# Kernel optimization log

Hardware: AMD Instinct MI355X
Metric: run time of the kernel (lower is better)

The kernel has to match this reference:

```python
import jax, jax.numpy as jnp
import numpy as np

D_MODEL = 2048
N_HEAD = 16
HEAD_DIM = D_MODEL // N_HEAD


def setup_inputs() -> dict:
    key = jax.random.key(0)
    k1, k2, k3 = jax.random.split(key, 3)
    B, T = 4, 1024
    x = jax.random.normal(k1, (B, T, D_MODEL), dtype=jnp.float32)
    # Linear(d_model, 3*d_model, bias=False): stored as [in, out] for x @ W
    w_qkv = jax.random.normal(k2, (D_MODEL, 3 * D_MODEL), dtype=jnp.float32) * (1.0 / np.sqrt(D_MODEL))
    w_proj = jax.random.normal(k3, (D_MODEL, D_MODEL), dtype=jnp.float32) * (1.0 / np.sqrt(D_MODEL))
    return {"x": x, "w_qkv": w_qkv, "w_proj": w_proj}


def reference(x, w_qkv, w_proj):
    B, T, C = x.shape
    H, Dh = N_HEAD, HEAD_DIM
    qkv = x @ w_qkv                              # [B, T, 3C]
    q, k, v = jnp.split(qkv, 3, axis=-1)
    # [B, T, C] -> [B, H, T, Dh]
    q = q.reshape(B, T, H, Dh).transpose(0, 2, 1, 3)
    k = k.reshape(B, T, H, Dh).transpose(0, 2, 1, 3)
    v = v.reshape(B, T, H, Dh).transpose(0, 2, 1, 3)
    scale = 1.0 / np.sqrt(Dh).astype(np.float32)
    scores = jnp.einsum('bhqd,bhkd->bhqk', q, k) * scale   # [B, H, T, T]
    causal = jnp.tril(jnp.ones((T, T), dtype=bool))
    scores = jnp.where(causal, scores, jnp.finfo(scores.dtype).min)
    attn = jax.nn.softmax(scores, axis=-1)
    y = jnp.einsum('bhqk,bhkd->bhqd', attn, v)             # [B, H, T, Dh]
    y = y.transpose(0, 2, 1, 3).reshape(B, T, C)
    return y @ w_proj
```

## Files before the change

### kernel.cpp

```cpp
#include <hip/hip_runtime.h>
#include <cstdint>
#include <cstddef>


typedef __attribute__((ext_vector_type(8))) __bf16 bf16x8;
typedef __attribute__((ext_vector_type(4))) float f32x4;
typedef unsigned short u16;

#define NEG_BIG (-1.0e30f)

__device__ __forceinline__ u16 f2bf(float f) {
    union { float f; uint32_t u; } v; v.f = f;
    uint32_t r = v.u + 0x7FFFu + ((v.u >> 16) & 1u);
    return (u16)(r >> 16);
}

__device__ __forceinline__ uint32_t pack2(float a, float b) {
    return (uint32_t)f2bf(a) | ((uint32_t)f2bf(b) << 16);
}

__device__ __forceinline__ f32x4 mfma16(bf16x8 a, bf16x8 b, f32x4 c) {
    return __builtin_amdgcn_mfma_f32_16x16x32_bf16(a, b, c, 0, 0, 0);
}

__device__ __forceinline__ void async16(const u16* g, u16* l) {
    __builtin_amdgcn_global_load_lds(
        (const __attribute__((address_space(1))) void*)g,
        (__attribute__((address_space(3))) void*)l, 16, 0, 0);
}

__global__ __launch_bounds__(256) void cvt_bf16(
    const float* __restrict__ x, u16* __restrict__ xb) {
    size_t i = ((size_t)blockIdx.x * 256 + threadIdx.x) * 8;
    float4 u = *(const float4*)(x + i);
    float4 v = *(const float4*)(x + i + 4);
    uint4 p;
    p.x = pack2(u.x, u.y); p.y = pack2(u.z, u.w);
    p.z = pack2(v.x, v.y); p.w = pack2(v.z, v.w);
    *(uint4*)(xb + i) = p;
}

__global__ __launch_bounds__(256) void transpose_w(
    const float* __restrict__ W, int ldW, u16* __restrict__ WT) {
    __shared__ u16 tile[64][68];
    const int n0 = blockIdx.x * 64, k0 = blockIdx.y * 64;
    const int t = threadIdx.x;
    for (int i = t; i < 4096; i += 256) {
        int r = i >> 6, c = i & 63;
        tile[r][c] = f2bf(W[(size_t)(k0 + r) * ldW + n0 + c]);
    }
    __syncthreads();
    for (int i = t; i < 4096; i += 256) {
        int r = i >> 6, c = i & 63;
        WT[(size_t)(n0 + r) * 2048 + k0 + c] = tile[c][r];
    }
}

__global__ __launch_bounds__(256) void gemm_k(
    const void* __restrict__ Av, const u16* __restrict__ Bt,
    int N, int amode, int omode,
    float* __restrict__ outf, u16* __restrict__ Qo, u16* __restrict__ Ko,
    u16* __restrict__ Vt) {
    const int K = 2048;
    __shared__ u16 As[128][32];
    __shared__ u16 Bs[128][32];

    const float* A32 = (const float*)Av;
    const u16*   A16 = (const u16*)Av;

    const int m0 = blockIdx.y * 128, n0 = blockIdx.x * 128;
    const int t = threadIdx.x;
    const int w = t >> 6, lane = t & 63;
    const int col = lane & 15, quad = lane >> 4;
    const int wrow = (w >> 1) * 64, wcol = (w & 1) * 64;

    f32x4 acc[4][4];
    #pragma unroll
    for (int i = 0; i < 4; ++i)
        #pragma unroll
        for (int j = 0; j < 4; ++j)
            acc[i][j] = (f32x4){0.f, 0.f, 0.f, 0.f};

    u16* as_flat = &As[0][0];
    u16* bs_flat = &Bs[0][0];
    const int c1 = (w << 6) | lane;
    const int c2 = c1 + 256;

    for (int k0 = 0; k0 < K; k0 += 32) {
        {
            const u16* g1 = Bt + (size_t)(n0 + (c1 >> 2)) * K + k0 + ((c1 & 3) << 3);
            async16(g1, bs_flat + (size_t)w * 512);
            const u16* g2 = Bt + (size_t)(n0 + (c2 >> 2)) * K + k0 + ((c2 & 3) << 3);
            async16(g2, bs_flat + 2048 + (size_t)w * 512);
        }
        if (amode == 2) {
            const u16* g1 = A16 + (size_t)(m0 + (c1 >> 2)) * K + k0 + ((c1 & 3) << 3);
            async16(g1, as_flat + (size_t)w * 512);
            const u16* g2 = A16 + (size_t)(m0 + (c2 >> 2)) * K + k0 + ((c2 & 3) << 3);
            async16(g2, as_flat + 2048 + (size_t)w * 512);
        } else if (amode == 1) {
            #pragma unroll
            for (int cc = 0; cc < 2; ++cc) {
                int c = cc ? c2 : c1;
                int r = c >> 2, ko = (c & 3) << 3;
                int kg = k0 + ko, h = kg >> 7, d = kg & 127;
                int m = m0 + r, b = m >> 10, tt = m & 1023;
                const u16* g = A16 + (((size_t)(b * 16 + h)) * 1024 + tt) * 128 + d;
                async16(g, as_flat + (size_t)(cc ? 2048 : 0) + (size_t)w * 512);
            }
        } else if (amode == 0) {
            #pragma unroll
            for (int c = t; c < 512; c += 256) {
                int r = c >> 2, ko = (c & 3) * 8;
                size_t off = (size_t)(m0 + r) * K + k0 + ko;
                float4 u = *(const float4*)(A32 + off);
                float4 v = *(const float4*)(A32 + off + 4);
                uint4 p;
                p.x = pack2(u.x, u.y); p.y = pack2(u.z, u.w);
                p.z = pack2(v.x, v.y); p.w = pack2(v.z, v.w);
                *(uint4*)&As[r][ko] = p;
            }
        } else {
            #pragma unroll
            for (int c = t; c < 512; c += 256) {
                int r = c >> 2, ko = (c & 3) * 8;
                int kg = k0 + ko, h = kg >> 7, d = kg & 127;
                int m = m0 + r, b = m >> 10, tt = m & 1023;
                *(uint4*)&As[r][ko] =
                    *(const uint4*)(A16 + (((size_t)(b * 16 + h)) * 1024 + tt) * 128 + d);
            }
        }
        __syncthreads();

        bf16x8 afr[4], bfr[4];
        #pragma unroll
        for (int i = 0; i < 4; ++i)
            afr[i] = *(const bf16x8*)&As[wrow + i * 16 + col][quad * 8];
        #pragma unroll
        for (int i = 0; i < 4; ++i)
            bfr[i] = *(const bf16x8*)&Bs[wcol + i * 16 + col][quad * 8];

        #pragma unroll
        for (int mt = 0; mt < 4; ++mt)
            #pragma unroll
            for (int nt = 0; nt < 4; ++nt)
                acc[mt][nt] = mfma16(afr[mt], bfr[nt], acc[mt][nt]);
        __syncthreads();
    }

    #pragma unroll
    for (int mt = 0; mt < 4; ++mt) {
        #pragma unroll
        for (int nt = 0; nt < 4; ++nt) {
            #pragma unroll
            for (int r = 0; r < 4; ++r) {
                int gm = m0 + wrow + mt * 16 + quad * 4 + r;
                int gn = n0 + wcol + nt * 16 + col;
                if (omode == 0) {
                    outf[(size_t)gm * N + gn] = acc[mt][nt][r];
                } else {
                    u16 bv = f2bf(acc[mt][nt][r]);
                    int b = gm >> 10, tq = gm & 1023;
                    if (omode == 3) {
                        int which = gn >> 11, rem = gn & 2047;
                        int h = rem >> 7, d = rem & 127;
                        size_t bh = (size_t)b * 16 + h;
                        if (which == 0)      Qo[(bh * 1024 + tq) * 128 + d] = bv;
                        else if (which == 1) Ko[(bh * 1024 + tq) * 128 + d] = bv;
                        else                 Vt[(bh * 128 + d) * 1024 + tq] = bv;
                    } else {
                        int h = gn >> 7, d = gn & 127;
                        size_t bh = (size_t)b * 16 + h;
                        if (omode == 1) Qo[(bh * 1024 + tq) * 128 + d] = bv;
                        else            Vt[(bh * 128 + d) * 1024 + tq] = bv;
                    }
                }
            }
        }
    }
}

__device__ __forceinline__ bf16x8 ldsfrag(const u16* buf, int row, int ksl, int quad) {
    return *(const bf16x8*)(buf + (size_t)row * 64 +
                            ((((ksl << 2) | quad) ^ (row & 7)) << 3));
}

template<int AMODE>
__device__ __forceinline__ void stageA(
    u16* halfb, const u16* A, int m0h, int k0, int w, int lane) {
    #pragma unroll
    for (int j = 0; j < 2; ++j) {
        int s0 = (j << 9) | (w << 6);
        int s = s0 + lane;
        int r = s >> 3;
        int gc = (s & 7) ^ (r & 7);
        int k = k0 + (gc << 3);
        const u16* src;
        if constexpr (AMODE == 2) {
            src = A + (size_t)(m0h + r) * 2048 + k;
        } else {
            int m = m0h + r, b = m >> 10, tt = m & 1023;
            int hh = k >> 7, d = k & 127;
            src = A + (((size_t)(b * 16 + hh)) * 1024 + tt) * 128 + d;
        }
        async16(src, halfb + (size_t)s0 * 8);
    }
}

__device__ __forceinline__ void stageB256(
    u16* halfb, const u16* Bt, int n0h, int k0, int w, int lane) {
    #pragma unroll
    for (int j = 0; j < 2; ++j) {
        int s0 = (j << 9) | (w << 6);
        int s = s0 + lane;
        int r = s >> 3;
        int gc = (s & 7) ^ (r & 7);
        async16(Bt + (size_t)(n0h + r) * 2048 + k0 + (gc << 3),
                halfb + (size_t)s0 * 8);
    }
}

template<int AMODE, int OMODE>
__global__ __launch_bounds__(512, 2) void gemm256(
    const u16* __restrict__ A, const u16* __restrict__ Bt, int N,
    float* __restrict__ outf, u16* __restrict__ Qo, u16* __restrict__ Ko,
    u16* __restrict__ Vt) {
    __shared__ u16 As[2][256 * 64];
    __shared__ u16 Bs[2][256 * 64];

    const int m0 = blockIdx.y * 256, n0 = blockIdx.x * 256;
    const int t = threadIdx.x;
    const int w = t >> 6, lane = t & 63;
    const int col = lane & 15, quad = lane >> 4;
    const int wr16 = ((w >> 2) & 1) << 4;
    const int wc16 = (w & 3) << 4;

    f32x4 acc[8][4];
    #pragma unroll
    for (int i = 0; i < 8; ++i)
        #pragma unroll
        for (int j = 0; j < 4; ++j)
            acc[i][j] = (f32x4){0.f, 0.f, 0.f, 0.f};

    stageA<AMODE>(As[0],             A,  m0,       0, w, lane);
    stageB256(    Bs[0],             Bt, n0,       0, w, lane);
    stageB256(    Bs[0] + 128 * 64,  Bt, n0 + 128, 0, w, lane);
    stageA<AMODE>(As[0] + 128 * 64,  A,  m0 + 128, 0, w, lane);
    asm volatile("s_waitcnt vmcnt(4)" ::: "memory");
    __builtin_amdgcn_s_barrier();

    const int NT = 2048 / 64;
    bf16x8 a_frag[8], b0_frag[4], b1_frag[4];

    for (int kt = 0; kt < NT; ++kt) {
        const int bt = kt & 1, bn = bt ^ 1;
        const int ktn = (kt + 1 < NT) ? kt + 1 : 0;
        const u16* asC = As[bt];
        const u16* bsC = Bs[bt];
        u16* asN = As[bn];
        u16* bsN = Bs[bn];
        const int kN = ktn * 64;

        #pragma unroll
        for (int mr = 0; mr < 4; ++mr)
            #pragma unroll
            for (int ks = 0; ks < 2; ++ks)
                a_frag[mr * 2 + ks] = ldsfrag(asC, mr * 32 + wr16 + col, ks, quad);
        #pragma unroll
        for (int nr = 0; nr < 2; ++nr)
            #pragma unroll
            for (int ks = 0; ks < 2; ++ks)
                b0_frag[nr * 2 + ks] = ldsfrag(bsC, nr * 64 + wc16 + col, ks, quad);
        stageA<AMODE>(asN, A, m0, kN, w, lane);
        asm volatile("s_waitcnt vmcnt(4)" ::: "memory");
        __builtin_amdgcn_s_barrier();
        __builtin_amdgcn_s_setprio(1);
        #pragma unroll
        for (int mr = 0; mr < 4; ++mr)
            #pragma unroll
            for (int nr = 0; nr < 2; ++nr)
                #pragma unroll
                for (int ks = 0; ks < 2; ++ks)
                    acc[mr][nr] = mfma16(a_frag[mr * 2 + ks], b0_frag[nr * 2 + ks], acc[mr][nr]);
        __builtin_amdgcn_s_setprio(0);

        #pragma unroll
        for (int nr = 0; nr < 2; ++nr)
            #pragma unroll
            for (int ks = 0; ks < 2; ++ks)
                b1_frag[nr * 2 + ks] = ldsfrag(bsC, (nr + 2) * 64 + wc16 + col, ks, quad);
        stageB256(bsN, Bt, n0, kN, w, lane);
        asm volatile("s_waitcnt vmcnt(4)" ::: "memory");
        __builtin_amdgcn_s_barrier();
        __builtin_amdgcn_s_setprio(1);
        #pragma unroll
        for (int mr = 0; mr < 4; ++mr)
            #pragma unroll
            for (int nr = 0; nr < 2; ++nr)
                #pragma unroll
                for (int ks = 0; ks < 2; ++ks)
                    acc[mr][nr + 2] = mfma16(a_frag[mr * 2 + ks], b1_frag[nr * 2 + ks], acc[mr][nr + 2]);
        __builtin_amdgcn_s_setprio(0);

        #pragma unroll
        for (int mr = 0; mr < 4; ++mr)
            #pragma unroll
            for (int ks = 0; ks < 2; ++ks)
                a_frag[mr * 2 + ks] = ldsfrag(asC, (mr + 4) * 32 + wr16 + col, ks, quad);
        stageB256(bsN + 128 * 64, Bt, n0 + 128, kN, w, lane);
        __builtin_amdgcn_s_barrier();
        __builtin_amdgcn_s_setprio(1);
        #pragma unroll
        for (int mr = 0; mr < 4; ++mr)
            #pragma unroll
            for (int nr = 0; nr < 2; ++nr)
                #pragma unroll
                for (int ks = 0; ks < 2; ++ks)
                    acc[mr + 4][nr + 2] = mfma16(a_frag[mr * 2 + ks], b1_frag[nr * 2 + ks], acc[mr + 4][nr + 2]);
        __builtin_amdgcn_s_setprio(0);

        stageA<AMODE>(asN + 128 * 64, A, m0 + 128, kN, w, lane);
        asm volatile("s_waitcnt vmcnt(4)" ::: "memory");
        __builtin_amdgcn_s_barrier();
        __builtin_amdgcn_s_setprio(1);
        #pragma unroll
        for (int mr = 0; mr < 4; ++mr)
            #pragma unroll
            for (int nr = 0; nr < 2; ++nr)
                #pragma unroll
                for (int ks = 0; ks < 2; ++ks)
                    acc[mr + 4][nr] = mfma16(a_frag[mr * 2 + ks], b0_frag[nr * 2 + ks], acc[mr + 4][nr]);
        __builtin_amdgcn_s_setprio(0);
    }

    #pragma unroll
    for (int mr = 0; mr < 8; ++mr) {
        #pragma unroll
        for (int nr = 0; nr < 4; ++nr) {
            #pragma unroll
            for (int r = 0; r < 4; ++r) {
                int gm = m0 + mr * 32 + wr16 + quad * 4 + r;
                int gn = n0 + nr * 64 + wc16 + col;
                if constexpr (OMODE == 0) {
                    outf[(size_t)gm * N + gn] = acc[mr][nr][r];
                } else {
                    u16 bv = f2bf(acc[mr][nr][r]);
                    int b = gm >> 10, tq = gm & 1023;
                    int which = gn >> 11, rem = gn & 2047;
                    int hh = rem >> 7, d = rem & 127;
                    size_t bh = (size_t)b * 16 + hh;
                    if (which == 0)      Qo[(bh * 1024 + tq) * 128 + d] = bv;
                    else if (which == 1) Ko[(bh * 1024 + tq) * 128 + d] = bv;
                    else                 Vt[(bh * 128 + d) * 1024 + tq] = bv;
                }
            }
        }
    }
}

__global__ __launch_bounds__(256) void attn_kernel(
    u16* __restrict__ Q, const u16* __restrict__ K,
    const u16* __restrict__ VT) {
    __shared__ u16 Ks[64 * 128];
    __shared__ u16 Vs[128 * 64];
    __shared__ u16 Ps[4][16][68];

    const int qb = (int)(gridDim.x - 1) - (int)blockIdx.x;
    const int h = blockIdx.y, b = blockIdx.z;
    const int t = threadIdx.x;
    const int w = t >> 6, lane = t & 63;
    const int col = lane & 15, quad = lane >> 4;
    const int sw = col & 7;
    const size_t bh = (size_t)b * 16 + h;
    u16* Qb = Q + bh * (1024 * 128);
    const u16* Kb = K + bh * (1024 * 128);
    const u16* Vb = VT + bh * (128 * 1024);
    const int q_lane = qb * 64 + w * 16 + col;

    bf16x8 qf[4];
    {
        const u16* qp = Qb + (size_t)q_lane * 128 + quad * 8;
        #pragma unroll
        for (int kq = 0; kq < 4; ++kq)
            qf[kq] = *(const bf16x8*)(qp + kq * 32);
    }

    f32x4 o[8];
    #pragma unroll
    for (int i = 0; i < 8; ++i) o[i] = (f32x4){0.f, 0.f, 0.f, 0.f};
    float m = NEG_BIG, l = 0.f;
    const float scale = 0.08838834764831845f;

    for (int kt = 0; kt <= qb; ++kt) {
        const u16* Kt = Kb + (size_t)kt * (64 * 128);

        #pragma unroll
        for (int i = 0; i < 4; ++i) {
            int s = i * 256 + w * 64 + lane;
            int kr = s >> 4, kc = s & 15;
            async16(Kt + (size_t)kr * 128 + ((kc ^ (kr & 7)) << 3),
                    Ks + (size_t)(i * 256 + w * 64) * 8);
            int vr = s >> 3, vc = s & 7;
            async16(Vb + (size_t)vr * 1024 + kt * 64 + ((vc ^ (vr & 7)) << 3),
                    Vs + (size_t)(i * 256 + w * 64) * 8);
        }
        __syncthreads();

        const bool need_mask = (kt == qb);
        const int ttmax = need_mask ? w : 3;
        f32x4 s[4];
        #pragma unroll
        for (int tt = 0; tt < 4; ++tt) {
            if (tt > ttmax) { s[tt] = (f32x4){NEG_BIG, NEG_BIG, NEG_BIG, NEG_BIG}; continue; }
            const u16* kbase = Ks + (size_t)(tt * 16 + col) * 128;
            f32x4 a = (f32x4){0.f, 0.f, 0.f, 0.f};
            #pragma unroll
            for (int kq = 0; kq < 4; ++kq)
                a = mfma16(*(const bf16x8*)(kbase + (((kq * 4 + quad) ^ sw) << 3)),
                           qf[kq], a);
            s[tt] = a;
        }

        float rmax = NEG_BIG;
        #pragma unroll
        for (int tt = 0; tt < 4; ++tt) {
            if (tt > ttmax) continue;
            #pragma unroll
            for (int r = 0; r < 4; ++r) {
                float v = s[tt][r] * scale;
                int tg = kt * 64 + tt * 16 + quad * 4 + r;
                if (need_mask && tg > q_lane) v = NEG_BIG;
                s[tt][r] = v;
                rmax = fmaxf(rmax, v);
            }
        }
        rmax = fmaxf(rmax, __shfl_xor(rmax, 16, 64));
        rmax = fmaxf(rmax, __shfl_xor(rmax, 32, 64));

        float mnew = fmaxf(m, rmax);
        float alpha = __expf(m - mnew);
        m = mnew;

        float rsum = 0.f;
        #pragma unroll
        for (int tt = 0; tt < 4; ++tt) {
            uint32_t* dst = (uint32_t*)&Ps[w][col][tt * 16 + quad * 4];
            if (tt > ttmax) { dst[0] = 0u; dst[1] = 0u; continue; }
            float p0 = __expf(s[tt][0] - mnew);
            float p1 = __expf(s[tt][1] - mnew);
            float p2 = __expf(s[tt][2] - mnew);
            float p3 = __expf(s[tt][3] - mnew);
            rsum += (p0 + p1) + (p2 + p3);
            dst[0] = pack2(p0, p1);
            dst[1] = pack2(p2, p3);
        }
        rsum += __shfl_xor(rsum, 16, 64);
        rsum += __shfl_xor(rsum, 32, 64);
        l = l * alpha + rsum;

        #pragma unroll
        for (int dt = 0; dt < 8; ++dt)
            #pragma unroll
            for (int r = 0; r < 4; ++r) o[dt][r] *= alpha;

        #pragma unroll
        for (int ks = 0; ks < 2; ++ks) {
            bf16x8 pf = *(const bf16x8*)&Ps[w][col][ks * 32 + quad * 8];
            #pragma unroll
            for (int dt = 0; dt < 8; ++dt) {
                const u16* vbase = Vs + (size_t)(dt * 16 + col) * 64;
                o[dt] = mfma16(*(const bf16x8*)(vbase + (((ks * 4 + quad) ^ sw) << 3)),
                               pf, o[dt]);
            }
        }
        __syncthreads();
    }

    float inv = 1.0f / l;
    #pragma unroll
    for (int dt = 0; dt < 8; ++dt) {
        uint2 p;
        p.x = pack2(o[dt][0] * inv, o[dt][1] * inv);
        p.y = pack2(o[dt][2] * inv, o[dt][3] * inv);
        *(uint2*)&Qb[(size_t)q_lane * 128 + dt * 16 + quad * 4] = p;
    }
}

extern "C" void kernel_launch(void* const* d_in, const int* in_sizes, int n_in,
                              void* d_out, int out_size, void* d_ws, size_t ws_size,
                              hipStream_t stream) {
    const float* x      = (const float*)d_in[0];
    const float* w_qkv  = (const float*)d_in[1];
    const float* w_proj = (const float*)d_in[2];
    float* out = (float*)d_out;

    const size_t SEG = (size_t)4 * 16 * 1024 * 128;
    const size_t NEED_FAST = ((size_t)6144 * 2048 + SEG * 4) * 2;

    if (ws_size >= NEED_FAST + (1u << 20)) {
        u16* wT = (u16*)d_ws;
        u16* xb = wT + (size_t)6144 * 2048;
        u16* Qb = xb + SEG;
        u16* Kb = Qb + SEG;
        u16* Vb = Kb + SEG;

        cvt_bf16<<<4096, 256, 0, stream>>>(x, xb);
        transpose_w<<<dim3(96, 32), 256, 0, stream>>>(w_qkv, 6144, wT);

        gemm256<2, 3><<<dim3(24, 16), 512, 0, stream>>>(xb, wT, 6144,
                                                        nullptr, Qb, Kb, Vb);

        attn_kernel<<<dim3(16, 16, 4), 256, 0, stream>>>(Qb, Kb, Vb);

        transpose_w<<<dim3(32, 32), 256, 0, stream>>>(w_proj, 2048, wT);
        gemm_k<<<dim3(16, 32), 256, 0, stream>>>(Qb, wT, 2048, 1, 0,
                                                 out, nullptr, nullptr, nullptr);
    } else {
        u16* wT = (u16*)d_ws;
        u16* Qb = wT + (size_t)2048 * 2048;
        u16* Kb = Qb + SEG;
        u16* Vb = Kb + SEG;

        transpose_w<<<dim3(32, 32), 256, 0, stream>>>(w_qkv + 0, 6144, wT);
        gemm_k<<<dim3(16, 32), 256, 0, stream>>>(x, wT, 2048, 0, 1,
                                                 nullptr, Qb, nullptr, nullptr);
        transpose_w<<<dim3(32, 32), 256, 0, stream>>>(w_qkv + 2048, 6144, wT);
        gemm_k<<<dim3(16, 32), 256, 0, stream>>>(x, wT, 2048, 0, 1,
                                                 nullptr, Kb, nullptr, nullptr);
        transpose_w<<<dim3(32, 32), 256, 0, stream>>>(w_qkv + 4096, 6144, wT);
        gemm_k<<<dim3(16, 32), 256, 0, stream>>>(x, wT, 2048, 0, 2,
                                                 nullptr, nullptr, nullptr, Vb);

        attn_kernel<<<dim3(16, 16, 4), 256, 0, stream>>>(Qb, Kb, Vb);

        transpose_w<<<dim3(32, 32), 256, 0, stream>>>(w_proj, 2048, wT);
        gemm_k<<<dim3(16, 32), 256, 0, stream>>>(Qb, wT, 2048, 3, 0,
                                                 out, nullptr, nullptr, nullptr);
    }
}
```

Measured before the change: 437.8 us.

## Restructure GEMM main loop into quarter-buffer ping-pong pipeline with deeper prefetch

Splits the LDS A/B tiles into 128-row halves and unrolls the K loop by two, with a 'zigzag' order of 8 MFMA quadrants per iteration. Each quadrant's shared-memory half is refilled by async loads as soon as it has been consumed. The prologue prefetches most of the next K tile, so more global loads stay in flight (vmcnt 6) and fewer stalls land on barriers. The risk is tricky hazards in buffer reuse, and the final B half seems to rely on wrap-around indexing.

```diff
diff --git a/kernel.cpp b/kernel.cpp
--- a/kernel.cpp
+++ b/kernel.cpp
@@ -185,6 +185,37 @@
                             ((((ksl << 2) | quad) ^ (row & 7)) << 3));
 }
 
+__device__ __forceinline__ void read_a(bf16x8* af, const u16* buf,
+                                       int wr16, int col, int quad) {
+    #pragma unroll
+    for (int mr = 0; mr < 4; ++mr)
+        #pragma unroll
+        for (int ks = 0; ks < 2; ++ks)
+            af[mr * 2 + ks] = ldsfrag(buf, mr * 32 + wr16 + col, ks, quad);
+}
+
+__device__ __forceinline__ void read_b(bf16x8* bf, const u16* buf,
+                                       int wc16, int col, int quad) {
+    #pragma unroll
+    for (int nr = 0; nr < 2; ++nr)
+        #pragma unroll
+        for (int ks = 0; ks < 2; ++ks)
+            bf[nr * 2 + ks] = ldsfrag(buf, nr * 64 + wc16 + col, ks, quad);
+}
+
+__device__ __forceinline__ void mfma8(f32x4 (&acc)[8][4], int mh, int nh,
+                                      const bf16x8* af, const bf16x8* bf) {
+    #pragma unroll
+    for (int mr = 0; mr < 4; ++mr)
+        #pragma unroll
+        for (int nr = 0; nr < 2; ++nr)
+            #pragma unroll
+            for (int ks = 0; ks < 2; ++ks)
+                acc[mh * 4 + mr][nh * 2 + nr] =
+                    mfma16(af[mr * 2 + ks], bf[nr * 2 + ks],
+                           acc[mh * 4 + mr][nh * 2 + nr]);
+}
+
 template<int AMODE>
 __device__ __forceinline__ void stageA(
     u16* halfb, const u16* A, int m0h, int k0, int w, int lane) {
@@ -225,8 +256,8 @@
     const u16* __restrict__ A, const u16* __restrict__ Bt, int N,
     float* __restrict__ outf, u16* __restrict__ Qo, u16* __restrict__ Ko,
     u16* __restrict__ Vt) {
-    __shared__ u16 As[2][256 * 64];
-    __shared__ u16 Bs[2][256 * 64];
+    __shared__ u16 As[2][2][128 * 64];
+    __shared__ u16 Bs[2][2][128 * 64];
 
     const int m0 = blockIdx.y * 256, n0 = blockIdx.x * 256;
     const int t = threadIdx.x;
@@ -242,94 +273,82 @@
         for (int j = 0; j < 4; ++j)
             acc[i][j] = (f32x4){0.f, 0.f, 0.f, 0.f};
 
-    stageA<AMODE>(As[0],             A,  m0,       0, w, lane);
-    stageB256(    Bs[0],             Bt, n0,       0, w, lane);
-    stageB256(    Bs[0] + 128 * 64,  Bt, n0 + 128, 0, w, lane);
-    stageA<AMODE>(As[0] + 128 * 64,  A,  m0 + 128, 0, w, lane);
-    asm volatile("s_waitcnt vmcnt(4)" ::: "memory");
+    stageA<AMODE>(As[0][0], A,  m0,       0,  w, lane);
+    stageB256(    Bs[0][1], Bt, n0 + 128, 0,  w, lane);
+    stageA<AMODE>(As[0][1], A,  m0 + 128, 0,  w, lane);
+    stageB256(    Bs[0][0], Bt, n0,       0,  w, lane);
+    stageA<AMODE>(As[1][0], A,  m0,       64, w, lane);
+    stageB256(    Bs[1][1], Bt, n0 + 128, 64, w, lane);
+    stageA<AMODE>(As[1][1], A,  m0 + 128, 64, w, lane);
+    asm volatile("s_waitcnt vmcnt(6)" ::: "memory");
     __builtin_amdgcn_s_barrier();
 
-    const int NT = 2048 / 64;
-    bf16x8 a_frag[8], b0_frag[4], b1_frag[4];
-
-    for (int kt = 0; kt < NT; ++kt) {
-        const int bt = kt & 1, bn = bt ^ 1;
-        const int ktn = (kt + 1 < NT) ? kt + 1 : 0;
-        const u16* asC = As[bt];
-        const u16* bsC = Bs[bt];
-        u16* asN = As[bn];
-        u16* bsN = Bs[bn];
-        const int kN = ktn * 64;
-
-        #pragma unroll
-        for (int mr = 0; mr < 4; ++mr)
-            #pragma unroll
-            for (int ks = 0; ks < 2; ++ks)
-                a_frag[mr * 2 + ks] = ldsfrag(asC, mr * 32 + wr16 + col, ks, quad);
-        #pragma unroll
-        for (int nr = 0; nr < 2; ++nr)
-            #pragma unroll
-            for (int ks = 0; ks < 2; ++ks)
-                b0_frag[nr * 2 + ks] = ldsfrag(bsC, nr * 64 + wc16 + col, ks, quad);
-        stageA<AMODE>(asN, A, m0, kN, w, lane);
-        asm volatile("s_waitcnt vmcnt(4)" ::: "memory");
-        __builtin_amdgcn_s_barrier();
-        __builtin_amdgcn_s_setprio(1);
-        #pragma unroll
-        for (int mr = 0; mr < 4; ++mr)
-            #pragma unroll
-            for (int nr = 0; nr < 2; ++nr)
-                #pragma unroll
-                for (int ks = 0; ks < 2; ++ks)
-                    acc[mr][nr] = mfma16(a_frag[mr * 2 + ks], b0_frag[nr * 2 + ks], acc[mr][nr]);
-        __builtin_amdgcn_s_setprio(0);
-
-        #pragma unroll
-        for (int nr = 0; nr < 2; ++nr)
-            #pragma unroll
-            for (int ks = 0; ks < 2; ++ks)
-                b1_frag[nr * 2 + ks] = ldsfrag(bsC, (nr + 2) * 64 + wc16 + col, ks, quad);
-        stageB256(bsN, Bt, n0, kN, w, lane);
-        asm volatile("s_waitcnt vmcnt(4)" ::: "memory");
-        __builtin_amdgcn_s_barrier();
-        __builtin_amdgcn_s_setprio(1);
-        #pragma unroll
-        for (int mr = 0; mr < 4; ++mr)
-            #pragma unroll
-            for (int nr = 0; nr < 2; ++nr)
-                #pragma unroll
-                for (int ks = 0; ks < 2; ++ks)
-                    acc[mr][nr + 2] = mfma16(a_frag[mr * 2 + ks], b1_frag[nr * 2 + ks], acc[mr][nr + 2]);
-        __builtin_amdgcn_s_setprio(0);
-
-        #pragma unroll
-        for (int mr = 0; mr < 4; ++mr)
-            #pragma unroll
-            for (int ks = 0; ks < 2; ++ks)
-                a_frag[mr * 2 + ks] = ldsfrag(asC, (mr + 4) * 32 + wr16 + col, ks, quad);
-        stageB256(bsN + 128 * 64, Bt, n0 + 128, kN, w, lane);
-        __builtin_amdgcn_s_barrier();
-        __builtin_amdgcn_s_setprio(1);
-        #pragma unroll
-        for (int mr = 0; mr < 4; ++mr)
-            #pragma unroll
-            for (int nr = 0; nr < 2; ++nr)
-                #pragma unroll
-                for (int ks = 0; ks < 2; ++ks)
-                    acc[mr + 4][nr + 2] = mfma16(a_frag[mr * 2 + ks], b1_frag[nr * 2 + ks], acc[mr + 4][nr + 2]);
-        __builtin_amdgcn_s_setprio(0);
-
-        stageA<AMODE>(asN + 128 * 64, A, m0 + 128, kN, w, lane);
-        asm volatile("s_waitcnt vmcnt(4)" ::: "memory");
-        __builtin_amdgcn_s_barrier();
-        __builtin_amdgcn_s_setprio(1);
-        #pragma unroll
-        for (int mr = 0; mr < 4; ++mr)
-            #pragma unroll
-            for (int nr = 0; nr < 2; ++nr)
-                #pragma unroll
-                for (int ks = 0; ks < 2; ++ks)
-                    acc[mr + 4][nr] = mfma16(a_frag[mr * 2 + ks], b0_frag[nr * 2 + ks], acc[mr + 4][nr]);
+    const int NIT = 16;
+    bf16x8 a_frag[8], b_frag[4];
+
+    for (int tt = 0; tt < NIT; ++tt) {
+        const int ka = (2 * tt + 1) & 31;
+        const int kb = (2 * tt + 2) & 31;
+        const int kc = (2 * tt + 3) & 31;
+
+        read_a(a_frag, As[0][0], wr16, col, quad);
+        read_b(b_frag, Bs[0][0], wc16, col, quad);
+        stageB256(Bs[1][0], Bt, n0, ka * 64, w, lane);
+        __builtin_amdgcn_s_barrier();
+        __builtin_amdgcn_s_setprio(1);
+        mfma8(acc, 0, 0, a_frag, b_frag);
+        __builtin_amdgcn_s_setprio(0);
+
+        read_b(b_frag, Bs[0][1], wc16, col, quad);
+        stageA<AMODE>(As[0][0], A, m0, kb * 64, w, lane);
+        __builtin_amdgcn_s_barrier();
+        __builtin_amdgcn_s_setprio(1);
+        mfma8(acc, 0, 1, a_frag, b_frag);
+        __builtin_amdgcn_s_setprio(0);
+
+        read_a(a_frag, As[0][1], wr16, col, quad);
+        stageB256(Bs[0][1], Bt, n0 + 128, kb * 64, w, lane);
+        __builtin_amdgcn_s_barrier();
+        __builtin_amdgcn_s_setprio(1);
+        mfma8(acc, 1, 1, a_frag, b_frag);
+        __builtin_amdgcn_s_setprio(0);
+
+        read_b(b_frag, Bs[0][0], wc16, col, quad);
+        stageA<AMODE>(As[0][1], A, m0 + 128, kb * 64, w, lane);
+        asm volatile("s_waitcnt vmcnt(6)" ::: "memory");
+        __builtin_amdgcn_s_barrier();
+        __builtin_amdgcn_s_setprio(1);
+        mfma8(acc, 1, 0, a_frag, b_frag);
+        __builtin_amdgcn_s_setprio(0);
+
+        read_a(a_frag, As[1][0], wr16, col, quad);
+        read_b(b_frag, Bs[1][0], wc16, col, quad);
+        stageB256(Bs[0][0], Bt, n0, kb * 64, w, lane);
+        __builtin_amdgcn_s_barrier();
+        __builtin_amdgcn_s_setprio(1);
+        mfma8(acc, 0, 0, a_frag, b_frag);
+        __builtin_amdgcn_s_setprio(0);
+
+        read_b(b_frag, Bs[1][1], wc16, col, quad);
+        stageA<AMODE>(As[1][0], A, m0, kc * 64, w, lane);
+        __builtin_amdgcn_s_barrier();
+        __builtin_amdgcn_s_setprio(1);
+        mfma8(acc, 0, 1, a_frag, b_frag);
+        __builtin_amdgcn_s_setprio(0);
+
+        read_a(a_frag, As[1][1], wr16, col, quad);
+        stageB256(Bs[1][1], Bt, n0 + 128, kc * 64, w, lane);
+        __builtin_amdgcn_s_barrier();
+        __builtin_amdgcn_s_setprio(1);
+        mfma8(acc, 1, 1, a_frag, b_frag);
+        __builtin_amdgcn_s_setprio(0);
+
+        read_b(b_frag, Bs[1][0], wc16, col, quad);
+        stageA<AMODE>(As[1][1], A, m0 + 128, kc * 64, w, lane);
+        asm volatile("s_waitcnt vmcnt(6)" ::: "memory");
+        __builtin_amdgcn_s_barrier();
+        __builtin_amdgcn_s_setprio(1);
+        mfma8(acc, 1, 0, a_frag, b_frag);
         __builtin_amdgcn_s_setprio(0);
     }
 
```

Measured after the change: 449.1 us. 1.03x slower.
